# Performance work log

Hardware: AMD Instinct MI355X
Metric: run time of the kernel (lower is better)

The kernel has to match this reference:

```python
import jax, jax.numpy as jnp
import numpy as np


def setup_inputs() -> dict:
    key = jax.random.key(0)
    k1, k2 = jax.random.split(key)
    B, H, W, D = 4096, 64, 64, 512
    inputs = jax.random.normal(k1, (B, D), dtype=jnp.float32)
    # keras 'random_uniform' initializer default range [-0.05, 0.05]
    weights_map = jax.random.uniform(k2, (H, W, D), dtype=jnp.float32,
                                     minval=-0.05, maxval=0.05)
    return {"inputs": inputs, "weights_map": weights_map}


def reference(inputs, weights_map):
    # inputs: (B, D); weights_map: (H, W, D)
    H, W, D = weights_map.shape
    flat_w = weights_map.reshape(-1, D)              # (N, D), N = H*W
    # avoids materializing the (B, N, D) difference tensor)
    x_sq = jnp.sum(inputs * inputs, axis=1, keepdims=True)    # (B, 1)
    w_sq = jnp.sum(flat_w * flat_w, axis=1)                   # (N,)
    sq_dist = x_sq - 2.0 * (inputs @ flat_w.T) + w_sq         # (B, N)
    sq_dist = jnp.maximum(sq_dist, 0.0)
    bmu_flat = jnp.argmin(sq_dist, axis=1)                    # (B,)
    bmu_y = (bmu_flat // W).astype(jnp.int32)
    bmu_x = (bmu_flat % W).astype(jnp.int32)
    bmu_indices = jnp.stack([bmu_y, bmu_x], axis=1)           # (B, 2)
    min_sq = jnp.take_along_axis(sq_dist, bmu_flat[:, None], axis=1)[:, 0]
    quantization_errors = jnp.sqrt(min_sq)                    # (B,)
    return bmu_indices, quantization_errors
```

## Files before the change

kernel.cpp:

```cpp
#include <hip/hip_runtime.h>

#define B_ROWS 4096
#define N_COLS 4096
#define DIM    512
#define LDK    1024

typedef __attribute__((ext_vector_type(8))) short short8;
typedef __attribute__((ext_vector_type(4))) float floatx4;

__device__ __forceinline__ unsigned short f2bf_rn(float f) {
    unsigned u = __float_as_uint(f);
    u += 0x7fffu + ((u >> 16) & 1u);
    return (unsigned short)(u >> 16);
}
__device__ __forceinline__ float bf2f(unsigned short h) {
    return __uint_as_float(((unsigned)h) << 16);
}

__device__ __forceinline__ unsigned long long pack_key(float v, int idx) {
    unsigned u = __float_as_uint(v);
    u = (u & 0x80000000u) ? ~u : (u | 0x80000000u);
    return ((unsigned long long)u << 32) | (unsigned)idx;
}

__device__ __forceinline__ void async16(const unsigned short* g, unsigned short* l) {
    __builtin_amdgcn_global_load_lds(
        (__attribute__((address_space(1))) void*)g,
        (__attribute__((address_space(3))) void*)l, 16, 0, 0);
}

__global__ __launch_bounds__(256) void som_convert(
    const float* __restrict__ X, const float* __restrict__ Wt,
    unsigned short* __restrict__ Xc, unsigned short* __restrict__ Wc,
    float* __restrict__ x_sq, float* __restrict__ w_sq,
    unsigned long long* __restrict__ packed)
{
    int wave = threadIdx.x >> 6, lane = threadIdx.x & 63;
    int grow = blockIdx.x * 4 + wave;
    bool isX = grow < B_ROWS;
    const float* src = isX ? (X + (size_t)grow * DIM)
                           : (Wt + (size_t)(grow - B_ROWS) * DIM);
    const float4* p4 = (const float4*)src;
    float4 a = p4[lane * 2], b = p4[lane * 2 + 1];
    float f[8] = {a.x, a.y, a.z, a.w, b.x, b.y, b.z, b.w};
    short8 hi, lo;
    float s = 0.f;
    #pragma unroll
    for (int t = 0; t < 8; ++t) {
        unsigned short h = f2bf_rn(f[t]);
        hi[t] = (short)h;
        lo[t] = (short)f2bf_rn(f[t] - bf2f(h));
        s = fmaf(f[t], f[t], s);
    }
    unsigned short* dst = (isX ? Xc + (size_t)grow * LDK
                               : Wc + (size_t)(grow - B_ROWS) * LDK) + lane * 8;
    *(short8*)(dst)       = hi;
    *(short8*)(dst + 512) = lo;
    #pragma unroll
    for (int off = 32; off >= 1; off >>= 1) s += __shfl_xor(s, off, 64);
    if (lane == 0) {
        if (isX) { x_sq[grow] = s; packed[grow] = ~0ull; }
        else     { w_sq[grow - B_ROWS] = s; }
    }
}

__global__ __launch_bounds__(256, 2) void som_dist_v8(
    const unsigned short* __restrict__ Xc, const unsigned short* __restrict__ Wc,
    const float* __restrict__ w_sq, unsigned long long* __restrict__ packed)
{
    __shared__ __align__(16) unsigned short L[2 * 16384];
    const int tid  = threadIdx.x;
    const int wave = tid >> 6, lane = tid & 63;
    const int wr = wave >> 1, wc = wave & 1;
    const int bm = blockIdx.y, bn = blockIdx.x;
    const int quad = lane >> 4, t16 = lane & 15;

    const int srow = lane >> 2;
    const int scol = ((((lane & 3) - ((lane >> 3) & 3)) & 3)) * 8;
    const unsigned short* gAh = Xc + (size_t)(bm * 128 + wave * 32 + srow) * LDK + scol;
    const unsigned short* gBh = Wc + (size_t)(bn * 128 + wave * 32 + srow) * LDK + scol;
    const unsigned short* gAl = gAh + 512;
    const unsigned short* gBl = gBh + 512;
    const int wofs = wave * 1024;

    const int rdw = 4 * t16 + ((quad + ((t16 >> 1) & 3)) & 3);
    const int ra = wr * 2048 + rdw * 8;
    const int rb = 8192 + wc * 2048 + rdw * 8;

    floatx4 acc[4][4];
    #pragma unroll
    for (int i = 0; i < 4; ++i)
        #pragma unroll
        for (int j = 0; j < 4; ++j) acc[i][j] = (floatx4){0.f, 0.f, 0.f, 0.f};

    #pragma unroll
    for (int b = 0; b < 2; ++b) {
        unsigned short* base = &L[b * 16384];
        const int k0 = b * 32;
        async16(gAh + k0,            base + wofs);
        async16(gAh + k0 + 16 * LDK, base + wofs + 512);
        async16(gAl + k0,            base + 4096 + wofs);
        async16(gAl + k0 + 16 * LDK, base + 4096 + wofs + 512);
        async16(gBh + k0,            base + 8192 + wofs);
        async16(gBh + k0 + 16 * LDK, base + 8192 + wofs + 512);
        async16(gBl + k0,            base + 12288 + wofs);
        async16(gBl + k0 + 16 * LDK, base + 12288 + wofs + 512);
    }

    #pragma unroll 1
    for (int kt = 0; kt < 16; ++kt) {
        const int cur = kt & 1;
        unsigned short* base = &L[cur * 16384];

        if (kt == 15) asm volatile("s_waitcnt vmcnt(0)" ::: "memory");
        else          asm volatile("s_waitcnt vmcnt(8)" ::: "memory");
        __builtin_amdgcn_s_barrier();

        short8 ah[4], bh[4], bl[4], al[4];
        #pragma unroll
        for (int i = 0; i < 4; ++i) ah[i] = *(const short8*)(base + ra + i * 512);
        #pragma unroll
        for (int j = 0; j < 4; ++j) bh[j] = *(const short8*)(base + rb + j * 512);

        __builtin_amdgcn_s_setprio(1);
        #pragma unroll
        for (int i = 0; i < 4; ++i)
            #pragma unroll
            for (int j = 0; j < 4; ++j)
                acc[i][j] = __builtin_amdgcn_mfma_f32_16x16x32_bf16(
                    ah[i], bh[j], acc[i][j], 0, 0, 0);
        __builtin_amdgcn_s_setprio(0);

        #pragma unroll
        for (int j = 0; j < 4; ++j) bl[j] = *(const short8*)(base + rb + 4096 + j * 512);
        #pragma unroll
        for (int i = 0; i < 4; ++i) al[i] = *(const short8*)(base + ra + 4096 + i * 512);

        asm volatile("s_waitcnt lgkmcnt(0)" ::: "memory");
        __builtin_amdgcn_s_barrier();

        if (kt < 14) {
            const int k0 = (kt + 2) * 32;
            async16(gAh + k0,            base + wofs);
            async16(gAh + k0 + 16 * LDK, base + wofs + 512);
            async16(gAl + k0,            base + 4096 + wofs);
            async16(gAl + k0 + 16 * LDK, base + 4096 + wofs + 512);
            async16(gBh + k0,            base + 8192 + wofs);
            async16(gBh + k0 + 16 * LDK, base + 8192 + wofs + 512);
            async16(gBl + k0,            base + 12288 + wofs);
            async16(gBl + k0 + 16 * LDK, base + 12288 + wofs + 512);
        }

        __builtin_amdgcn_s_setprio(1);
        #pragma unroll
        for (int i = 0; i < 4; ++i)
            #pragma unroll
            for (int j = 0; j < 4; ++j)
                acc[i][j] = __builtin_amdgcn_mfma_f32_16x16x32_bf16(
                    ah[i], bl[j], acc[i][j], 0, 0, 0);
        #pragma unroll
        for (int i = 0; i < 4; ++i)
            #pragma unroll
            for (int j = 0; j < 4; ++j)
                acc[i][j] = __builtin_amdgcn_mfma_f32_16x16x32_bf16(
                    al[i], bh[j], acc[i][j], 0, 0, 0);
        __builtin_amdgcn_s_setprio(0);
    }

    const int col0 = bn * 128 + wc * 64 + t16;
    float wq[4];
    #pragma unroll
    for (int j = 0; j < 4; ++j) wq[j] = w_sq[col0 + j * 16];
    const int row_base = bm * 128 + wr * 64 + quad * 4;
    #pragma unroll
    for (int i = 0; i < 4; ++i) {
        #pragma unroll
        for (int r = 0; r < 4; ++r) {
            unsigned long long best = ~0ull;
            #pragma unroll
            for (int j = 0; j < 4; ++j) {
                float val = fmaf(-2.f, acc[i][j][r], wq[j]);
                unsigned long long key = pack_key(val, col0 + j * 16);
                best = (key < best) ? key : best;
            }
            #pragma unroll
            for (int m = 1; m <= 8; m <<= 1) {
                unsigned long long o = __shfl_xor(best, m, 64);
                best = (o < best) ? o : best;
            }
            if (t16 == 0)
                atomicMin(&packed[row_base + i * 16 + r], best);
        }
    }
}

__global__ __launch_bounds__(256) void som_finalize(
    const unsigned long long* __restrict__ packed,
    const float* __restrict__ x_sq, float* __restrict__ out)
{
    int b = blockIdx.x * 256 + threadIdx.x;
    unsigned long long p = packed[b];
    unsigned idx = (unsigned)(p & 0xffffffffull);
    unsigned key = (unsigned)(p >> 32);
    unsigned u = (key & 0x80000000u) ? (key & 0x7fffffffu) : ~key;
    float val = __uint_as_float(u);
    float sq = fmaxf(x_sq[b] + val, 0.f);
    out[2 * b]     = (float)(idx >> 6);
    out[2 * b + 1] = (float)(idx & 63);
    out[2 * B_ROWS + b] = sqrtf(sq);
}

extern "C" void kernel_launch(void* const* d_in, const int* in_sizes, int n_in,
                              void* d_out, int out_size, void* d_ws, size_t ws_size,
                              hipStream_t stream) {
    const float* X  = (const float*)d_in[0];
    const float* Wt = (const float*)d_in[1];
    float* out = (float*)d_out;

    unsigned long long* packed = (unsigned long long*)d_ws;
    float* x_sq = (float*)((char*)d_ws + (32 << 10));
    float* w_sq = (float*)((char*)d_ws + (48 << 10));
    unsigned short* Xc = (unsigned short*)((char*)d_ws + (64 << 10));
    unsigned short* Wc = (unsigned short*)((char*)d_ws + (64 << 10) + ((size_t)B_ROWS * LDK * 2));

    som_convert<<<dim3((B_ROWS + N_COLS) / 4), dim3(256), 0, stream>>>(
        X, Wt, Xc, Wc, x_sq, w_sq, packed);
    som_dist_v8<<<dim3(N_COLS / 128, B_ROWS / 128), dim3(256), 0, stream>>>(
        Xc, Wc, w_sq, packed);
    som_finalize<<<dim3(B_ROWS / 256), dim3(256), 0, stream>>>(packed, x_sq, out);
}
```

Measured before the change: 127.5 us.

## Enlarge GEMM block tile to 256x256 with 8x8 MFMA fragments per wave

Each block's output tile grows from 128x128 to 256x256, so each wave now holds an 8x8 grid of 16x16 accumulators. The LDS double buffer doubles in size and the hi/lo split halves are interleaved per row group. The aim is more reuse of each loaded fragment and less global and LDS traffic per FLOP. In exchange, accumulator register pressure rises sharply (256 VGPRs of accumulators) and occupancy drops to one block per CU. The grid shrinks to 256 blocks, which may leave CUs underused on a 256-CU part.

```diff
diff --git a/kernel.cpp b/kernel.cpp
--- a/kernel.cpp
+++ b/kernel.cpp
@@ -64,121 +64,113 @@
     }
 }
 
-__global__ __launch_bounds__(256, 2) void som_dist_v8(
+#define MFMA64(AF, BF)                                          \
+    _Pragma("unroll")                                           \
+    for (int i = 0; i < 8; ++i)                                 \
+        _Pragma("unroll")                                       \
+        for (int j = 0; j < 8; ++j)                             \
+            acc[i][j] = __builtin_amdgcn_mfma_f32_16x16x32_bf16( \
+                AF[i], BF[j], acc[i][j], 0, 0, 0);
+
+__global__ __launch_bounds__(256, 1) void som_dist_v10(
     const unsigned short* __restrict__ Xc, const unsigned short* __restrict__ Wc,
     const float* __restrict__ w_sq, unsigned long long* __restrict__ packed)
 {
-    __shared__ __align__(16) unsigned short L[2 * 16384];
+    __shared__ __align__(16) unsigned short L[2 * 32768];
     const int tid  = threadIdx.x;
     const int wave = tid >> 6, lane = tid & 63;
+    const int quad = lane >> 4, t16 = lane & 15;
     const int wr = wave >> 1, wc = wave & 1;
     const int bm = blockIdx.y, bn = blockIdx.x;
-    const int quad = lane >> 4, t16 = lane & 15;
 
     const int srow = lane >> 2;
     const int scol = ((((lane & 3) - ((lane >> 3) & 3)) & 3)) * 8;
-    const unsigned short* gAh = Xc + (size_t)(bm * 128 + wave * 32 + srow) * LDK + scol;
-    const unsigned short* gBh = Wc + (size_t)(bn * 128 + wave * 32 + srow) * LDK + scol;
-    const unsigned short* gAl = gAh + 512;
-    const unsigned short* gBl = gBh + 512;
-    const int wofs = wave * 1024;
-
-    const int rdw = 4 * t16 + ((quad + ((t16 >> 1) & 3)) & 3);
-    const int ra = wr * 2048 + rdw * 8;
-    const int rb = 8192 + wc * 2048 + rdw * 8;
-
-    floatx4 acc[4][4];
-    #pragma unroll
-    for (int i = 0; i < 4; ++i)
-        #pragma unroll
-        for (int j = 0; j < 4; ++j) acc[i][j] = (floatx4){0.f, 0.f, 0.f, 0.f};
+    const unsigned short* gA = Xc + (size_t)(bm * 256 + wave * 64 + srow) * LDK + scol;
+    const unsigned short* gB = Wc + (size_t)(bn * 256 + wave * 64 + srow) * LDK + scol;
+    const int wofsA = wave * 8 * 512;
+    const int wofsB = 16384 + wave * 8 * 512;
+
+    const int rdw8 = (4 * t16 + ((quad + ((t16 >> 1) & 3)) & 3)) * 8;
+    const unsigned short* const pAb = &L[wr * 8192 + rdw8];
+    const unsigned short* const pBb = &L[16384 + wc * 8192 + rdw8];
+
+    floatx4 acc[8][8];
+    #pragma unroll
+    for (int i = 0; i < 8; ++i)
+        #pragma unroll
+        for (int j = 0; j < 8; ++j) acc[i][j] = (floatx4){0.f, 0.f, 0.f, 0.f};
 
     #pragma unroll
     for (int b = 0; b < 2; ++b) {
-        unsigned short* base = &L[b * 16384];
+        unsigned short* base = &L[b * 32768];
         const int k0 = b * 32;
-        async16(gAh + k0,            base + wofs);
-        async16(gAh + k0 + 16 * LDK, base + wofs + 512);
-        async16(gAl + k0,            base + 4096 + wofs);
-        async16(gAl + k0 + 16 * LDK, base + 4096 + wofs + 512);
-        async16(gBh + k0,            base + 8192 + wofs);
-        async16(gBh + k0 + 16 * LDK, base + 8192 + wofs + 512);
-        async16(gBl + k0,            base + 12288 + wofs);
-        async16(gBl + k0 + 16 * LDK, base + 12288 + wofs + 512);
+        #pragma unroll
+        for (int q = 0; q < 4; ++q) {
+            async16(gA + k0 + q * 16 * LDK,       base + wofsA + q * 1024);
+            async16(gA + k0 + q * 16 * LDK + 512, base + wofsA + q * 1024 + 512);
+            async16(gB + k0 + q * 16 * LDK,       base + wofsB + q * 1024);
+            async16(gB + k0 + q * 16 * LDK + 512, base + wofsB + q * 1024 + 512);
+        }
     }
 
     #pragma unroll 1
     for (int kt = 0; kt < 16; ++kt) {
         const int cur = kt & 1;
-        unsigned short* base = &L[cur * 16384];
 
         if (kt == 15) asm volatile("s_waitcnt vmcnt(0)" ::: "memory");
-        else          asm volatile("s_waitcnt vmcnt(8)" ::: "memory");
+        else          asm volatile("s_waitcnt vmcnt(16)" ::: "memory");
         __builtin_amdgcn_s_barrier();
 
-        short8 ah[4], bh[4], bl[4], al[4];
-        #pragma unroll
-        for (int i = 0; i < 4; ++i) ah[i] = *(const short8*)(base + ra + i * 512);
-        #pragma unroll
-        for (int j = 0; j < 4; ++j) bh[j] = *(const short8*)(base + rb + j * 512);
+        const unsigned short* pA = pAb + cur * 32768;
+        const unsigned short* pB = pBb + cur * 32768;
+        short8 ah[8], bh[8], bl[8], al[8];
+        #pragma unroll
+        for (int i = 0; i < 8; ++i) ah[i] = *(const short8*)(pA + i * 1024);
+        #pragma unroll
+        for (int j = 0; j < 8; ++j) bh[j] = *(const short8*)(pB + j * 1024);
 
         __builtin_amdgcn_s_setprio(1);
-        #pragma unroll
-        for (int i = 0; i < 4; ++i)
-            #pragma unroll
-            for (int j = 0; j < 4; ++j)
-                acc[i][j] = __builtin_amdgcn_mfma_f32_16x16x32_bf16(
-                    ah[i], bh[j], acc[i][j], 0, 0, 0);
+        MFMA64(ah, bh)
         __builtin_amdgcn_s_setprio(0);
 
         #pragma unroll
-        for (int j = 0; j < 4; ++j) bl[j] = *(const short8*)(base + rb + 4096 + j * 512);
-        #pragma unroll
-        for (int i = 0; i < 4; ++i) al[i] = *(const short8*)(base + ra + 4096 + i * 512);
+        for (int j = 0; j < 8; ++j) bl[j] = *(const short8*)(pB + j * 1024 + 512);
+        #pragma unroll
+        for (int i = 0; i < 8; ++i) al[i] = *(const short8*)(pA + i * 1024 + 512);
 
         asm volatile("s_waitcnt lgkmcnt(0)" ::: "memory");
         __builtin_amdgcn_s_barrier();
 
         if (kt < 14) {
+            unsigned short* base = &L[cur * 32768];
             const int k0 = (kt + 2) * 32;
-            async16(gAh + k0,            base + wofs);
-            async16(gAh + k0 + 16 * LDK, base + wofs + 512);
-            async16(gAl + k0,            base + 4096 + wofs);
-            async16(gAl + k0 + 16 * LDK, base + 4096 + wofs + 512);
-            async16(gBh + k0,            base + 8192 + wofs);
-            async16(gBh + k0 + 16 * LDK, base + 8192 + wofs + 512);
-            async16(gBl + k0,            base + 12288 + wofs);
-            async16(gBl + k0 + 16 * LDK, base + 12288 + wofs + 512);
+            #pragma unroll
+            for (int q = 0; q < 4; ++q) {
+                async16(gA + k0 + q * 16 * LDK,       base + wofsA + q * 1024);
+                async16(gA + k0 + q * 16 * LDK + 512, base + wofsA + q * 1024 + 512);
+                async16(gB + k0 + q * 16 * LDK,       base + wofsB + q * 1024);
+                async16(gB + k0 + q * 16 * LDK + 512, base + wofsB + q * 1024 + 512);
+            }
         }
 
         __builtin_amdgcn_s_setprio(1);
-        #pragma unroll
-        for (int i = 0; i < 4; ++i)
-            #pragma unroll
-            for (int j = 0; j < 4; ++j)
-                acc[i][j] = __builtin_amdgcn_mfma_f32_16x16x32_bf16(
-                    ah[i], bl[j], acc[i][j], 0, 0, 0);
-        #pragma unroll
-        for (int i = 0; i < 4; ++i)
-            #pragma unroll
-            for (int j = 0; j < 4; ++j)
-                acc[i][j] = __builtin_amdgcn_mfma_f32_16x16x32_bf16(
-                    al[i], bh[j], acc[i][j], 0, 0, 0);
+        MFMA64(ah, bl)
+        MFMA64(al, bh)
         __builtin_amdgcn_s_setprio(0);
     }
 
-    const int col0 = bn * 128 + wc * 64 + t16;
-    float wq[4];
-    #pragma unroll
-    for (int j = 0; j < 4; ++j) wq[j] = w_sq[col0 + j * 16];
-    const int row_base = bm * 128 + wr * 64 + quad * 4;
-    #pragma unroll
-    for (int i = 0; i < 4; ++i) {
+    const int col0 = bn * 256 + wc * 128 + t16;
+    float wq[8];
+    #pragma unroll
+    for (int j = 0; j < 8; ++j) wq[j] = w_sq[col0 + j * 16];
+    const int row_base = bm * 256 + wr * 128 + quad * 4;
+    #pragma unroll
+    for (int i = 0; i < 8; ++i) {
         #pragma unroll
         for (int r = 0; r < 4; ++r) {
             unsigned long long best = ~0ull;
             #pragma unroll
-            for (int j = 0; j < 4; ++j) {
+            for (int j = 0; j < 8; ++j) {
                 float val = fmaf(-2.f, acc[i][j][r], wq[j]);
                 unsigned long long key = pack_key(val, col0 + j * 16);
                 best = (key < best) ? key : best;
@@ -225,7 +217,7 @@
 
     som_convert<<<dim3((B_ROWS + N_COLS) / 4), dim3(256), 0, stream>>>(
         X, Wt, Xc, Wc, x_sq, w_sq, packed);
-    som_dist_v8<<<dim3(N_COLS / 128, B_ROWS / 128), dim3(256), 0, stream>>>(
+    som_dist_v10<<<dim3(N_COLS / 256, B_ROWS / 256), dim3(256), 0, stream>>>(
         Xc, Wc, w_sq, packed);
     som_finalize<<<dim3(B_ROWS / 256), dim3(256), 0, stream>>>(packed, x_sq, out);
 }
```

Measured after the change: 147.5 us. 15.7% more time.
